# Performance work log

Measured on AMD Instinct MI355X. Metric: run time of the kernel, lower is better.

Reference implementation:

```python
import jax, jax.numpy as jnp
import numpy as np

N_LAT, N_LON = 721, 1440
N_MESH = 40962
C_IN, N_FEAT = 64, 4
HID, OUT = 256, 256
BATCH = 2


def _precompute_interp(mesh_lat, mesh_lon):
    """Vectorized version of BilinearInterpolator.__init__ precompute."""
    lat_min, lon_min = -np.pi / 2, 0.0
    dlat = np.pi / (N_LAT - 1)
    dlon = 2 * np.pi / N_LON
    lon = np.mod(mesh_lon - lon_min, 2 * np.pi) + lon_min
    lat_idx = (mesh_lat - lat_min) / dlat
    lon_idx = (lon - lon_min) / dlon
    i0 = np.clip(np.floor(lat_idx).astype(np.int64), 0, N_LAT - 2)
    j0 = np.clip(np.floor(lon_idx).astype(np.int64), 0, N_LON - 2)
    i1 = i0 + 1
    j1 = (j0 + 1) % N_LON
    lf = np.clip(lat_idx - i0, 0.0, 1.0)
    jf = np.clip(lon_idx - j0, 0.0, 1.0)
    idx = np.stack([i0 * N_LON + j0, i0 * N_LON + j1,
                    i1 * N_LON + j0, i1 * N_LON + j1], axis=1)
    w = np.stack([(1 - lf) * (1 - jf), (1 - lf) * jf,
                  lf * (1 - jf), lf * jf], axis=1).astype(np.float32)
    return idx, w


def setup_inputs() -> dict:
    key = jax.random.key(0)
    k = jax.random.split(key, 6)
    rng = np.random.default_rng(0)
    mesh_lat = rng.uniform(-np.pi / 2 + 1e-3, np.pi / 2 - 1e-3, N_MESH)
    mesh_lon = rng.uniform(0.0, 2 * np.pi, N_MESH)
    idx, w = _precompute_interp(mesh_lat, mesh_lon)
    d_in = C_IN + N_FEAT
    return {
        "grid_data": jax.random.normal(k[0], (BATCH, N_LAT, N_LON, C_IN), jnp.float32),
        "mesh_features": jax.random.normal(k[1], (N_MESH, N_FEAT), jnp.float32),
        "indices": jnp.asarray(idx, jnp.int64 if jax.config.read('jax_enable_x64') else jnp.int32),
        "weights": jnp.asarray(w),
        "W1": jax.random.normal(k[2], (d_in, HID), jnp.float32) / np.sqrt(d_in),
        "b1": jnp.zeros((HID,), jnp.float32),
        "W2": jax.random.normal(k[3], (HID, OUT), jnp.float32) / np.sqrt(HID),
        "b2": jnp.zeros((OUT,), jnp.float32),
    }


def reference(grid_data, mesh_features, indices, weights, W1, b1, W2, b2):
    B, n_lat, n_lon, C = grid_data.shape
    grid_flat = grid_data.reshape(B, n_lat * n_lon, C)          # (B, G, C)
    corner = grid_flat[:, indices, :]                           # (B, M, 4, C)
    mesh_data = jnp.einsum('bmkc,mk->bmc', corner, weights)     # weighted 4-pt sum
    mf = jnp.broadcast_to(mesh_features[None], (B,) + mesh_features.shape)
    combined = jnp.concatenate([mesh_data, mf], axis=-1)        # (B, M, C+F)
    h = jax.nn.relu(combined @ W1 + b1)                         # 2-layer MLP
    return h @ W2 + b2                                          # (B, M, OUT)
```

## Files before the change

kernel.cpp:

```cpp
#include <hip/hip_runtime.h>
#include <hip/hip_bf16.h>


constexpr int kNLat  = 721;
constexpr int kNLon  = 1440;
constexpr long long kNPix = (long long)kNLat * kNLon;
constexpr int kMesh  = 40962;
constexpr int kCIn   = 64;
constexpr int kFeat  = 4;
constexpr int kDIn   = kCIn + kFeat;
constexpr int kHid   = 256;
constexpr int kOut   = 256;
constexpr int kBatch = 2;

constexpr int kPts    = kBatch * kMesh;
constexpr int kPtsPad = (kPts + 63) & ~63;
constexpr int KP      = 96;

typedef __attribute__((ext_vector_type(8))) short bf16x8;
typedef __attribute__((ext_vector_type(4))) float f32x4;

constexpr int    WSA1_N   = 16 * 3 * 64 * 8;
constexpr int    WSB2_N   = 16 * 8 * 64 * 8;
constexpr size_t COMB_OFF = WSA1_N + WSB2_N;
constexpr size_t COMB_N   = (size_t)kPtsPad * KP;
constexpr size_t WS_SPLIT_BYTES = (COMB_OFF + COMB_N) * 2;
constexpr size_t WS_FUSED_BYTES = COMB_OFF * 2;

__device__ inline ushort f2b(float v) {
    __hip_bfloat16 h = __float2bfloat16(v);
    return *reinterpret_cast<ushort*>(&h);
}

__global__ __launch_bounds__(256)
void g2m_prep(const float* __restrict__ W1, const float* __restrict__ W2,
              ushort* __restrict__ ws) {
    const int tid = blockIdx.x * 256 + threadIdx.x;
    if (tid < 3072) {
        const int l  = tid & 63;
        const int g  = tid >> 6;
        const int ks = g % 3;
        const int rt = g / 3;
        const int hid = rt * 16 + (l & 15);
        const int k0  = ks * 32 + (l >> 4) * 8;
        ushort tmp[8];
        #pragma unroll
        for (int j = 0; j < 8; ++j) {
            const int k = k0 + j;
            tmp[j] = f2b(k < kDIn ? W1[(size_t)k * kHid + hid] : 0.f);
        }
        *reinterpret_cast<bf16x8*>(ws + (size_t)tid * 8) =
            *reinterpret_cast<bf16x8*>(tmp);
    } else if (tid < 11264) {
        const int q  = tid - 3072;
        const int l  = q & 63;
        const int g  = q >> 6;
        const int ks = g % 8;
        const int ct = g / 8;
        const int col = ct * 16 + (l & 15);
        const int k0  = ks * 32 + (l >> 4) * 8;
        ushort tmp[8];
        #pragma unroll
        for (int j = 0; j < 8; ++j) {
            const int k = k0 + j;
            tmp[j] = f2b(W2[(size_t)k * kOut + col]);
        }
        *reinterpret_cast<bf16x8*>(ws + (size_t)(WSA1_N + q * 8)) =
            *reinterpret_cast<bf16x8*>(tmp);
    }
}

__global__ __launch_bounds__(256)
void g2m_gather(const float* __restrict__ grid,
                const float* __restrict__ mfeat,
                const int*   __restrict__ indices,
                const float* __restrict__ weights,
                ushort* __restrict__ comb) {
    const int lane = threadIdx.x & 63;
    const int wid  = (blockIdx.x * 256 + threadIdx.x) >> 6;
    const int nw   = (gridDim.x * 256) >> 6;

    for (int p = wid; p < kPtsPad; p += nw) {
        float v = 0.f, mf = 0.f;
        if (p < kPts) {
            const int b = p / kMesh;
            const int m = p - b * kMesh;
            const int4   id = *reinterpret_cast<const int4*>(indices + (size_t)m * 4);
            const float4 wt = *reinterpret_cast<const float4*>(weights + (size_t)m * 4);
            const float* gb = grid + (size_t)b * (size_t)(kNPix * kCIn);
            v = fmaf(wt.x, gb[(size_t)id.x * kCIn + lane],
                fmaf(wt.y, gb[(size_t)id.y * kCIn + lane],
                fmaf(wt.z, gb[(size_t)id.z * kCIn + lane],
                     wt.w * gb[(size_t)id.w * kCIn + lane])));
            if (lane < kFeat) mf = mfeat[(size_t)m * kFeat + lane];
        }
        ushort* row = comb + (size_t)p * KP;
        row[lane] = f2b(v);
        if (lane < kFeat) row[kCIn + lane] = f2b(mf);
        if (lane < KP - kDIn) row[kDIn + lane] = 0;
    }
}

constexpr int MP    = 64;
constexpr int NBLKB = kPtsPad / MP;
constexpr int HSTR  = 264;

__global__ __launch_bounds__(256)
void g2m_mlp(const ushort* __restrict__ comb,
             const float* __restrict__ b1,
             const float* __restrict__ b2,
             const ushort* __restrict__ ws,
             float* __restrict__ out)
{
    __shared__ __align__(16) ushort hbuf[MP * HSTR];

    const int t    = threadIdx.x;
    const int lane = t & 63;
    const int w    = t >> 6;
    const int p0   = blockIdx.x * MP;
    const int l15  = lane & 15;
    const int l4   = lane >> 4;

    {
        f32x4 acc1[4][4];
        #pragma unroll
        for (int r = 0; r < 4; ++r)
            #pragma unroll
            for (int mt = 0; mt < 4; ++mt) acc1[r][mt] = (f32x4)0.f;

        #pragma unroll
        for (int ks = 0; ks < 3; ++ks) {
            bf16x8 af[4], bfr[4];
            #pragma unroll
            for (int r = 0; r < 4; ++r) {
                const int rt = w * 4 + r;
                af[r] = *reinterpret_cast<const bf16x8*>(
                            ws + (size_t)((rt * 3 + ks) * 64 + lane) * 8);
            }
            #pragma unroll
            for (int mt = 0; mt < 4; ++mt)
                bfr[mt] = *reinterpret_cast<const bf16x8*>(
                            comb + (size_t)(p0 + mt * 16 + l15) * KP + ks * 32 + l4 * 8);
            #pragma unroll
            for (int r = 0; r < 4; ++r)
                #pragma unroll
                for (int mt = 0; mt < 4; ++mt)
                    acc1[r][mt] = __builtin_amdgcn_mfma_f32_16x16x32_bf16(
                                      af[r], bfr[mt], acc1[r][mt], 0, 0, 0);
        }

        #pragma unroll
        for (int r = 0; r < 4; ++r) {
            const int hid0 = (w * 4 + r) * 16 + l4 * 4;
            const float4 bv = *reinterpret_cast<const float4*>(b1 + hid0);
            #pragma unroll
            for (int mt = 0; mt < 4; ++mt) {
                const int m = mt * 16 + l15;
                ushort4 hv;
                hv.x = f2b(fmaxf(acc1[r][mt][0] + bv.x, 0.f));
                hv.y = f2b(fmaxf(acc1[r][mt][1] + bv.y, 0.f));
                hv.z = f2b(fmaxf(acc1[r][mt][2] + bv.z, 0.f));
                hv.w = f2b(fmaxf(acc1[r][mt][3] + bv.w, 0.f));
                *reinterpret_cast<ushort4*>(&hbuf[m * HSTR + hid0]) = hv;
            }
        }
    }
    __syncthreads();

    {
        f32x4 acc2[4][4];
        #pragma unroll
        for (int mt = 0; mt < 4; ++mt)
            #pragma unroll
            for (int c = 0; c < 4; ++c) acc2[mt][c] = (f32x4)0.f;

        #pragma unroll
        for (int ks = 0; ks < 8; ++ks) {
            bf16x8 af[4], bfr[4];
            #pragma unroll
            for (int mt = 0; mt < 4; ++mt)
                af[mt] = *reinterpret_cast<const bf16x8*>(
                            &hbuf[(mt * 16 + l15) * HSTR + ks * 32 + l4 * 8]);
            #pragma unroll
            for (int c = 0; c < 4; ++c) {
                const int ct = w * 4 + c;
                bfr[c] = *reinterpret_cast<const bf16x8*>(
                            ws + (size_t)(WSA1_N + ((ct * 8 + ks) * 64 + lane) * 8));
            }
            #pragma unroll
            for (int mt = 0; mt < 4; ++mt)
                #pragma unroll
                for (int c = 0; c < 4; ++c)
                    acc2[mt][c] = __builtin_amdgcn_mfma_f32_16x16x32_bf16(
                                      af[mt], bfr[c], acc2[mt][c], 0, 0, 0);
        }

        #pragma unroll
        for (int c = 0; c < 4; ++c) {
            const int ct  = w * 4 + c;
            const int col = ct * 16 + l15;
            const float bb = b2[col];
            #pragma unroll
            for (int mt = 0; mt < 4; ++mt) {
                const int ploc = p0 + mt * 16 + l4 * 4;
                #pragma unroll
                for (int r = 0; r < 4; ++r) {
                    const int p = ploc + r;
                    if (p < kPts)
                        out[(size_t)p * kOut + col] = acc2[mt][c][r] + bb;
                }
            }
        }
    }
}

constexpr int FNBLK = (kMesh + MP - 1) / MP;
constexpr int CSTR  = 104;

__global__ __launch_bounds__(256)
void g2m_mfma(const float* __restrict__ grid,
              const float* __restrict__ mfeat,
              const int*   __restrict__ indices,
              const float* __restrict__ weights,
              const float* __restrict__ b1,
              const float* __restrict__ b2,
              const ushort* __restrict__ ws,
              float* __restrict__ out)
{
    __shared__ __align__(16) ushort comb[MP * CSTR];
    __shared__ __align__(16) ushort hbuf[MP * HSTR];

    const int t    = threadIdx.x;
    const int lane = t & 63;
    const int w    = t >> 6;
    const int b    = blockIdx.y;
    const int m0   = blockIdx.x * MP;
    const int l15  = lane & 15;
    const int l4   = lane >> 4;

    {
        const int c = lane;
        const float* gb = grid + (size_t)b * (size_t)(kNPix * kCIn);
        #pragma unroll 4
        for (int pass = 0; pass < MP / 4; ++pass) {
            const int p = pass * 4 + w;
            const int m = m0 + p;
            float v = 0.f, mf = 0.f;
            if (m < kMesh) {
                const int4   id = *reinterpret_cast<const int4*>(indices + (size_t)m * 4);
                const float4 wt = *reinterpret_cast<const float4*>(weights + (size_t)m * 4);
                v = fmaf(wt.x, gb[(size_t)id.x * kCIn + c],
                    fmaf(wt.y, gb[(size_t)id.y * kCIn + c],
                    fmaf(wt.z, gb[(size_t)id.z * kCIn + c],
                         wt.w * gb[(size_t)id.w * kCIn + c])));
                if (c < kFeat) mf = mfeat[(size_t)m * kFeat + c];
            }
            comb[p * CSTR + c] = f2b(v);
            if (c < kFeat) comb[p * CSTR + kCIn + c] = f2b(mf);
            if (c < CSTR - kDIn) comb[p * CSTR + kDIn + c] = 0;
        }
    }
    __syncthreads();

    {
        f32x4 acc1[4][4];
        #pragma unroll
        for (int r = 0; r < 4; ++r)
            #pragma unroll
            for (int mt = 0; mt < 4; ++mt) acc1[r][mt] = (f32x4)0.f;

        #pragma unroll
        for (int ks = 0; ks < 3; ++ks) {
            bf16x8 af[4], bfr[4];
            #pragma unroll
            for (int r = 0; r < 4; ++r) {
                const int rt = w * 4 + r;
                af[r] = *reinterpret_cast<const bf16x8*>(
                            ws + (size_t)((rt * 3 + ks) * 64 + lane) * 8);
            }
            #pragma unroll
            for (int mt = 0; mt < 4; ++mt)
                bfr[mt] = *reinterpret_cast<const bf16x8*>(
                            &comb[(mt * 16 + l15) * CSTR + ks * 32 + l4 * 8]);
            #pragma unroll
            for (int r = 0; r < 4; ++r)
                #pragma unroll
                for (int mt = 0; mt < 4; ++mt)
                    acc1[r][mt] = __builtin_amdgcn_mfma_f32_16x16x32_bf16(
                                      af[r], bfr[mt], acc1[r][mt], 0, 0, 0);
        }

        #pragma unroll
        for (int r = 0; r < 4; ++r) {
            const int hid0 = (w * 4 + r) * 16 + l4 * 4;
            const float4 bv = *reinterpret_cast<const float4*>(b1 + hid0);
            #pragma unroll
            for (int mt = 0; mt < 4; ++mt) {
                const int m = mt * 16 + l15;
                ushort4 hv;
                hv.x = f2b(fmaxf(acc1[r][mt][0] + bv.x, 0.f));
                hv.y = f2b(fmaxf(acc1[r][mt][1] + bv.y, 0.f));
                hv.z = f2b(fmaxf(acc1[r][mt][2] + bv.z, 0.f));
                hv.w = f2b(fmaxf(acc1[r][mt][3] + bv.w, 0.f));
                *reinterpret_cast<ushort4*>(&hbuf[m * HSTR + hid0]) = hv;
            }
        }
    }
    __syncthreads();

    {
        f32x4 acc2[4][4];
        #pragma unroll
        for (int mt = 0; mt < 4; ++mt)
            #pragma unroll
            for (int c = 0; c < 4; ++c) acc2[mt][c] = (f32x4)0.f;

        #pragma unroll
        for (int ks = 0; ks < 8; ++ks) {
            bf16x8 af[4], bfr[4];
            #pragma unroll
            for (int mt = 0; mt < 4; ++mt)
                af[mt] = *reinterpret_cast<const bf16x8*>(
                            &hbuf[(mt * 16 + l15) * HSTR + ks * 32 + l4 * 8]);
            #pragma unroll
            for (int c = 0; c < 4; ++c) {
                const int ct = w * 4 + c;
                bfr[c] = *reinterpret_cast<const bf16x8*>(
                            ws + (size_t)(WSA1_N + ((ct * 8 + ks) * 64 + lane) * 8));
            }
            #pragma unroll
            for (int mt = 0; mt < 4; ++mt)
                #pragma unroll
                for (int c = 0; c < 4; ++c)
                    acc2[mt][c] = __builtin_amdgcn_mfma_f32_16x16x32_bf16(
                                      af[mt], bfr[c], acc2[mt][c], 0, 0, 0);
        }

        #pragma unroll
        for (int c = 0; c < 4; ++c) {
            const int ct  = w * 4 + c;
            const int col = ct * 16 + l15;
            const float bb = b2[col];
            #pragma unroll
            for (int mt = 0; mt < 4; ++mt) {
                const int mloc = mt * 16 + l4 * 4;
                #pragma unroll
                for (int r = 0; r < 4; ++r) {
                    const int m = m0 + mloc + r;
                    if (m < kMesh)
                        out[((size_t)b * kMesh + m) * kOut + col] = acc2[mt][c][r] + bb;
                }
            }
        }
    }
}

extern "C" void kernel_launch(void* const* d_in, const int* in_sizes, int n_in,
                              void* d_out, int out_size, void* d_ws, size_t ws_size,
                              hipStream_t stream) {
    const float* grid    = (const float*)d_in[0];
    const float* mfeat   = (const float*)d_in[1];
    const int*   indices = (const int*)d_in[2];
    const float* weights = (const float*)d_in[3];
    const float* W1      = (const float*)d_in[4];
    const float* b1      = (const float*)d_in[5];
    const float* W2      = (const float*)d_in[6];
    const float* b2      = (const float*)d_in[7];
    float* o = (float*)d_out;

    if (ws_size >= WS_SPLIT_BYTES) {
        ushort* ws   = (ushort*)d_ws;
        ushort* comb = ws + COMB_OFF;
        g2m_prep<<<44, 256, 0, stream>>>(W1, W2, ws);
        g2m_gather<<<2048, 256, 0, stream>>>(grid, mfeat, indices, weights, comb);
        g2m_mlp<<<NBLKB, 256, 0, stream>>>(comb, b1, b2, ws, o);
    } else if (ws_size >= WS_FUSED_BYTES) {
        ushort* ws = (ushort*)d_ws;
        g2m_prep<<<44, 256, 0, stream>>>(W1, W2, ws);
        dim3 grd(FNBLK, kBatch);
        g2m_mfma<<<grd, 256, 0, stream>>>(grid, mfeat, indices, weights, b1, b2, ws, o);
    }
}
```

Before: 62.33 us.

## Fuse weight prep into gather, vectorize gather loads, transpose MFMA for float4 stores

The weight-conversion prep kernel is folded into the gather kernel, which removes one launch. The gather now has each 16-lane group handle one point with float4 loads and ushort4 stores over a fixed 3-iteration loop. The second MLP GEMM swaps its MFMA operands so that each lane holds four consecutive output columns, which allows float4 output stores and float4 bias loads. A risk is that the fused prep runs in the same kernel as the gather, although the MLP still depends only on the gather kernel finishing.

```diff
diff --git a/kernel.cpp b/kernel.cpp
--- a/kernel.cpp
+++ b/kernel.cpp
@@ -32,10 +32,9 @@
     return *reinterpret_cast<ushort*>(&h);
 }
 
-__global__ __launch_bounds__(256)
-void g2m_prep(const float* __restrict__ W1, const float* __restrict__ W2,
-              ushort* __restrict__ ws) {
-    const int tid = blockIdx.x * 256 + threadIdx.x;
+__device__ inline void prep_body(int tid, const float* __restrict__ W1,
+                                 const float* __restrict__ W2,
+                                 ushort* __restrict__ ws) {
     if (tid < 3072) {
         const int l  = tid & 63;
         const int g  = tid >> 6;
@@ -71,33 +70,63 @@
 }
 
 __global__ __launch_bounds__(256)
+void g2m_prep(const float* __restrict__ W1, const float* __restrict__ W2,
+              ushort* __restrict__ ws) {
+    prep_body(blockIdx.x * 256 + threadIdx.x, W1, W2, ws);
+}
+
+constexpr int NGB = 1708;
+
+__global__ __launch_bounds__(256)
 void g2m_gather(const float* __restrict__ grid,
                 const float* __restrict__ mfeat,
                 const int*   __restrict__ indices,
                 const float* __restrict__ weights,
-                ushort* __restrict__ comb) {
+                const float* __restrict__ W1,
+                const float* __restrict__ W2,
+                ushort* __restrict__ ws) {
+    const int tid = blockIdx.x * 256 + threadIdx.x;
+    if (tid < 11264) prep_body(tid, W1, W2, ws);
+
+    ushort* comb = ws + COMB_OFF;
     const int lane = threadIdx.x & 63;
-    const int wid  = (blockIdx.x * 256 + threadIdx.x) >> 6;
-    const int nw   = (gridDim.x * 256) >> 6;
-
-    for (int p = wid; p < kPtsPad; p += nw) {
-        float v = 0.f, mf = 0.f;
+    const int l15  = lane & 15;
+    const int q    = lane >> 4;
+    const int wid  = tid >> 6;
+    const int nw   = NGB * 4;
+
+    #pragma unroll
+    for (int it = 0; it < 3; ++it) {
+        const int g = wid + it * nw;
+        const int p = g * 4 + q;
+        float4 acc = {0.f, 0.f, 0.f, 0.f};
+        float mf0 = 0.f, mf1 = 0.f;
         if (p < kPts) {
-            const int b = p / kMesh;
+            const int b = (p >= kMesh) ? 1 : 0;
             const int m = p - b * kMesh;
             const int4   id = *reinterpret_cast<const int4*>(indices + (size_t)m * 4);
             const float4 wt = *reinterpret_cast<const float4*>(weights + (size_t)m * 4);
             const float* gb = grid + (size_t)b * (size_t)(kNPix * kCIn);
-            v = fmaf(wt.x, gb[(size_t)id.x * kCIn + lane],
-                fmaf(wt.y, gb[(size_t)id.y * kCIn + lane],
-                fmaf(wt.z, gb[(size_t)id.z * kCIn + lane],
-                     wt.w * gb[(size_t)id.w * kCIn + lane])));
-            if (lane < kFeat) mf = mfeat[(size_t)m * kFeat + lane];
+            const float4 r0 = *reinterpret_cast<const float4*>(gb + (size_t)id.x * kCIn + l15 * 4);
+            const float4 r1 = *reinterpret_cast<const float4*>(gb + (size_t)id.y * kCIn + l15 * 4);
+            const float4 r2 = *reinterpret_cast<const float4*>(gb + (size_t)id.z * kCIn + l15 * 4);
+            const float4 r3 = *reinterpret_cast<const float4*>(gb + (size_t)id.w * kCIn + l15 * 4);
+            acc.x = fmaf(wt.x, r0.x, fmaf(wt.y, r1.x, fmaf(wt.z, r2.x, wt.w * r3.x)));
+            acc.y = fmaf(wt.x, r0.y, fmaf(wt.y, r1.y, fmaf(wt.z, r2.y, wt.w * r3.y)));
+            acc.z = fmaf(wt.x, r0.z, fmaf(wt.y, r1.z, fmaf(wt.z, r2.z, wt.w * r3.z)));
+            acc.w = fmaf(wt.x, r0.w, fmaf(wt.y, r1.w, fmaf(wt.z, r2.w, wt.w * r3.w)));
+            if (l15 < 2) {
+                mf0 = mfeat[(size_t)m * kFeat + l15 * 2];
+                mf1 = mfeat[(size_t)m * kFeat + l15 * 2 + 1];
+            }
         }
         ushort* row = comb + (size_t)p * KP;
-        row[lane] = f2b(v);
-        if (lane < kFeat) row[kCIn + lane] = f2b(mf);
-        if (lane < KP - kDIn) row[kDIn + lane] = 0;
+        ushort4 pk;
+        pk.x = f2b(acc.x); pk.y = f2b(acc.y); pk.z = f2b(acc.z); pk.w = f2b(acc.w);
+        *reinterpret_cast<ushort4*>(row + l15 * 4) = pk;
+        ushort2 ft;
+        ft.x = f2b(mf0); ft.y = f2b(mf1);
+        *reinterpret_cast<ushort2*>(row + 64 + l15 * 2) = ft;
     }
 }
 
@@ -176,15 +205,15 @@
 
         #pragma unroll
         for (int ks = 0; ks < 8; ++ks) {
-            bf16x8 af[4], bfr[4];
-            #pragma unroll
-            for (int mt = 0; mt < 4; ++mt)
-                af[mt] = *reinterpret_cast<const bf16x8*>(
+            bf16x8 hf[4], wf[4];
+            #pragma unroll
+            for (int mt = 0; mt < 4; ++mt)
+                hf[mt] = *reinterpret_cast<const bf16x8*>(
                             &hbuf[(mt * 16 + l15) * HSTR + ks * 32 + l4 * 8]);
             #pragma unroll
             for (int c = 0; c < 4; ++c) {
                 const int ct = w * 4 + c;
-                bfr[c] = *reinterpret_cast<const bf16x8*>(
+                wf[c] = *reinterpret_cast<const bf16x8*>(
                             ws + (size_t)(WSA1_N + ((ct * 8 + ks) * 64 + lane) * 8));
             }
             #pragma unroll
@@ -192,22 +221,23 @@
                 #pragma unroll
                 for (int c = 0; c < 4; ++c)
                     acc2[mt][c] = __builtin_amdgcn_mfma_f32_16x16x32_bf16(
-                                      af[mt], bfr[c], acc2[mt][c], 0, 0, 0);
+                                      wf[c], hf[mt], acc2[mt][c], 0, 0, 0);
         }
 
         #pragma unroll
         for (int c = 0; c < 4; ++c) {
-            const int ct  = w * 4 + c;
-            const int col = ct * 16 + l15;
-            const float bb = b2[col];
+            const int col0 = (w * 4 + c) * 16 + l4 * 4;
+            const float4 bv = *reinterpret_cast<const float4*>(b2 + col0);
             #pragma unroll
             for (int mt = 0; mt < 4; ++mt) {
-                const int ploc = p0 + mt * 16 + l4 * 4;
-                #pragma unroll
-                for (int r = 0; r < 4; ++r) {
-                    const int p = ploc + r;
-                    if (p < kPts)
-                        out[(size_t)p * kOut + col] = acc2[mt][c][r] + bb;
+                const int p = p0 + mt * 16 + l15;
+                if (p < kPts) {
+                    float4 o;
+                    o.x = acc2[mt][c][0] + bv.x;
+                    o.y = acc2[mt][c][1] + bv.y;
+                    o.z = acc2[mt][c][2] + bv.z;
+                    o.w = acc2[mt][c][3] + bv.w;
+                    *reinterpret_cast<float4*>(out + (size_t)p * kOut + col0) = o;
                 }
             }
         }
@@ -371,8 +401,7 @@
     if (ws_size >= WS_SPLIT_BYTES) {
         ushort* ws   = (ushort*)d_ws;
         ushort* comb = ws + COMB_OFF;
-        g2m_prep<<<44, 256, 0, stream>>>(W1, W2, ws);
-        g2m_gather<<<2048, 256, 0, stream>>>(grid, mfeat, indices, weights, comb);
+        g2m_gather<<<NGB, 256, 0, stream>>>(grid, mfeat, indices, weights, W1, W2, ws);
         g2m_mlp<<<NBLKB, 256, 0, stream>>>(comb, b1, b2, ws, o);
     } else if (ws_size >= WS_FUSED_BYTES) {
         ushort* ws = (ushort*)d_ws;
```

New measurement: 54.31 us. 1.15x faster.
